# Kernel optimization log

Hardware: AMD Instinct MI355X
Metric: run time of the kernel (lower is better)

Reference implementation:

```python
import jax, jax.numpy as jnp
import numpy as np

B, S, DIM, H = 2, 1024, 512, 8
HD = DIM // H          # head_dim = 64
EPS = 1e-5
W_SCALE = 0.02         # keep activations stable (relu(gate)^2 downstream)


def causal_fft_conv(filters, x):
    """filters: [S, H]; x: [b, h, s, d]. Linear (full) convolution along s,
    truncated to the first s samples — identical to
    jax.scipy.signal.convolve(filter, seq, method='fft')[:s] per (h, d)."""
    s = x.shape[2]
    n = 2 * s  # >= 2s-1, enough for linear convolution
    f = jnp.fft.rfft(filters.T, n=n, axis=-1)          # [h, nf]
    xf = jnp.fft.rfft(x, n=n, axis=2)                  # [b, h, nf, d]
    y = jnp.fft.irfft(xf * f[None, :, :, None], n=n, axis=2)
    return y[:, :, :s, :]


def setup_inputs() -> dict:
    key = jax.random.key(0)
    ks = jax.random.split(key, 8)
    inp = {
        "x": jax.random.normal(ks[0], (B, S, DIM), dtype=jnp.float32),
        "spectral_basis": jax.random.normal(ks[1], (S, H), dtype=jnp.float32),
        "wq_w": jax.random.normal(ks[2], (DIM, DIM), dtype=jnp.float32) * W_SCALE,
        "wq_b": jnp.zeros((DIM,), jnp.float32),
        "wk_w": jax.random.normal(ks[3], (DIM, DIM), dtype=jnp.float32) * W_SCALE,
        "wk_b": jnp.zeros((DIM,), jnp.float32),
        "wv_w": jax.random.normal(ks[4], (DIM, DIM), dtype=jnp.float32) * W_SCALE,
        "wv_b": jnp.zeros((DIM,), jnp.float32),
        "wo_w": jax.random.normal(ks[5], (DIM, DIM), dtype=jnp.float32) * W_SCALE,
        "wo_b": jnp.zeros((DIM,), jnp.float32),
        "gate_w": jax.random.normal(ks[6], (HD * HD, 1), dtype=jnp.float32) * W_SCALE,
        "gate_b": jnp.zeros((1,), jnp.float32),
    }
    return inp


def reference(x, spectral_basis, wq_w, wq_b, wk_w, wk_b, wv_w, wv_b,
              wo_w, wo_b, gate_w, gate_b):
    b, s, dim = x.shape
    h = spectral_basis.shape[1]
    hd = dim // h

    def proj(w, bias):
        return (x @ w + bias).reshape(b, s, h, hd).transpose(0, 2, 1, 3)  # [b,h,s,d]

    q = proj(wq_w, wq_b)
    k = proj(wk_w, wk_b) / jnp.sqrt(jnp.asarray(hd, x.dtype))
    v = proj(wv_w, wv_b)

    k = causal_fft_conv(spectral_basis, k)
    v = causal_fft_conv(spectral_basis, v)

    # Outer-product state per step: [b, h, s, d, e]
    Z = jnp.einsum('bhsd,bhse->bhsde', v, k)

    # gate_proj: Dense(1) over flattened (d, e)
    gl = jnp.einsum('bhsde,de->bhs', Z, gate_w.reshape(hd, hd)) + gate_b[0]
    gates = jax.nn.relu(gl) ** 2 + EPS                 # [b, h, s]
    gates = gates[..., None, None]                     # [b, h, s, 1, 1]

    # Associative scan with (+, +) == cumulative sums along s
    cum_gZ = jnp.cumsum(gates * Z, axis=2)             # [b, h, s, d, e]
    cum_g = jnp.cumsum(gates, axis=2)                  # [b, h, s, 1, 1]
    attn = cum_gZ / (cum_g + EPS)

    out = jnp.einsum('bhsd,bhsde->bhse', q, attn)      # [b, h, s, e]
    nrm = jnp.linalg.norm(out, axis=3, keepdims=True)
    out = out / jnp.maximum(nrm, EPS)
    out = out.transpose(0, 2, 1, 3).reshape(b, s, dim)
    return out @ wo_w + wo_b
```

## Files before the change

kernel.cpp:

```cpp
#include <hip/hip_runtime.h>
#include <math.h>

#define B 2
#define S 1024
#define DIM 512
#define H 8
#define HD 64
#define EPS 1e-5f

typedef __attribute__((ext_vector_type(8))) short bf16x8;
typedef __attribute__((ext_vector_type(4))) float f32x4;
typedef unsigned short u16;

__device__ inline u16 f2bf(float f) {
    unsigned int u = __float_as_uint(f);
    return (u16)((u + 0x7FFF + ((u >> 16) & 1)) >> 16);
}
__device__ inline float bf2f(u16 v) {
    return __uint_as_float(((unsigned int)v) << 16);
}
__device__ inline void split2(float x, u16* hi, u16* lo) {
    u16 h = f2bf(x);
    *hi = h;
    *lo = f2bf(x - bf2f(h));
}
#define MFMA16(a, b, c) __builtin_amdgcn_mfma_f32_16x16x32_bf16((a), (b), (c), 0, 0, 0)

__global__ void xconv_k(const float* __restrict__ x, u16* __restrict__ xh, u16* __restrict__ xl) {
    int i = blockIdx.x * 256 + threadIdx.x;
    float4 v = ((const float4*)x)[i];
    ushort4 h, l;
    split2(v.x, &h.x, &l.x); split2(v.y, &h.y, &l.y);
    split2(v.z, &h.z, &l.z); split2(v.w, &h.w, &l.w);
    ((ushort4*)xh)[i] = h; ((ushort4*)xl)[i] = l;
}

__global__ void wconv_k(const float* __restrict__ wq, const float* __restrict__ wk,
                        const float* __restrict__ wv, const float* __restrict__ wo,
                        u16* __restrict__ wqkvh, u16* __restrict__ wqkvl,
                        u16* __restrict__ woh, u16* __restrict__ wol) {
    int z = blockIdx.z;
    const float* src = (z == 0) ? wq : (z == 1) ? wk : (z == 2) ? wv : wo;
    u16* dh = (z < 3) ? (wqkvh + (size_t)z * 512 * 512) : woh;
    u16* dl = (z < 3) ? (wqkvl + (size_t)z * 512 * 512) : wol;
    int k0 = blockIdx.x * 64, n0 = blockIdx.y * 64;
    int tid = threadIdx.x;
    __shared__ float T[64][65];
    #pragma unroll
    for (int p = 0; p < 16; ++p) {
        int i = tid + 256 * p; int r = i >> 6, c = i & 63;
        T[r][c] = src[(k0 + r) * 512 + n0 + c];
    }
    __syncthreads();
    #pragma unroll
    for (int p = 0; p < 16; ++p) {
        int i = tid + 256 * p; int r = i >> 6, c = i & 63;
        size_t di = (size_t)(n0 + r) * 512 + k0 + c;
        split2(T[c][r], &dh[di], &dl[di]);
    }
}

__global__ void toep_build(const float* __restrict__ filt,
                           u16* __restrict__ Th, u16* __restrict__ Tl) {
    int h = blockIdx.x, delta = blockIdx.y;
    int tid = threadIdx.x;
    size_t base = ((size_t)h * 16 + delta) << 12;
    #pragma unroll
    for (int p = 0; p < 16; ++p) {
        int i = tid + 256 * p;
        int t = i >> 6, s = i & 63;
        int idx = delta * 64 + t - s;
        float v = (idx >= 0 && idx < S) ? filt[idx * H + h] : 0.f;
        split2(v, &Th[base + i], &Tl[base + i]);
    }
}

__global__ void zero_k(float* __restrict__ a) {
    int i = blockIdx.x * 256 + threadIdx.x;
    ((float4*)a)[i] = make_float4(0.f, 0.f, 0.f, 0.f);
}

__global__ void qkv_gemm(const u16* __restrict__ Ah, const u16* __restrict__ Al,
                         const u16* __restrict__ Bh, const u16* __restrict__ Bl,
                         const float* __restrict__ bq, const float* __restrict__ bk,
                         const float* __restrict__ bv,
                         u16* __restrict__ qh, u16* __restrict__ ql,
                         u16* __restrict__ kth, u16* __restrict__ ktl,
                         u16* __restrict__ vth, u16* __restrict__ vtl) {
    const int K = 512;
    __shared__ __align__(16) u16 Ash[64][72], Asl[64][72], Bsh[64][72], Bsl[64][72];
    int tid = threadIdx.x, w = tid >> 6, l = tid & 63;
    int m0 = blockIdx.x * 64, n0 = blockIdx.y * 64;
    f32x4 acc[4] = {};
    for (int k0 = 0; k0 < K; k0 += 64) {
        #pragma unroll
        for (int p = 0; p < 2; ++p) {
            int i = tid + 256 * p; int r = i >> 3, c8 = (i & 7) * 8;
            *(bf16x8*)&Ash[r][c8] = *(const bf16x8*)&Ah[(size_t)(m0 + r) * K + k0 + c8];
            *(bf16x8*)&Asl[r][c8] = *(const bf16x8*)&Al[(size_t)(m0 + r) * K + k0 + c8];
            *(bf16x8*)&Bsh[r][c8] = *(const bf16x8*)&Bh[(size_t)(n0 + r) * K + k0 + c8];
            *(bf16x8*)&Bsl[r][c8] = *(const bf16x8*)&Bl[(size_t)(n0 + r) * K + k0 + c8];
        }
        __syncthreads();
        #pragma unroll
        for (int kc = 0; kc < 2; ++kc) {
            int ar = 16 * w + (l & 15), ac = kc * 32 + (l >> 4) * 8;
            bf16x8 ah = *(const bf16x8*)&Ash[ar][ac];
            bf16x8 al = *(const bf16x8*)&Asl[ar][ac];
            #pragma unroll
            for (int cf = 0; cf < 4; ++cf) {
                int br = cf * 16 + (l & 15);
                bf16x8 bh_ = *(const bf16x8*)&Bsh[br][ac];
                bf16x8 bl_ = *(const bf16x8*)&Bsl[br][ac];
                acc[cf] = MFMA16(ah, bh_, acc[cf]);
                acc[cf] = MFMA16(ah, bl_, acc[cf]);
                acc[cf] = MFMA16(al, bh_, acc[cf]);
            }
        }
        __syncthreads();
    }
    #pragma unroll
    for (int cf = 0; cf < 4; ++cf) {
        #pragma unroll
        for (int r = 0; r < 4; ++r) {
            int m = m0 + 16 * w + 4 * (l >> 4) + r;
            int n = n0 + 16 * cf + (l & 15);
            int bb = m >> 10, s = m & 1023;
            int which = n >> 9, nn = n & 511;
            int hh = nn >> 6, d = nn & 63;
            int bh = bb * 8 + hh;
            float val = acc[cf][r];
            if (which == 0) {
                val += bq[nn];
                size_t di = ((size_t)bh * 1024 + s) * 64 + d;
                split2(val, &qh[di], &ql[di]);
            } else if (which == 1) {
                val = (val + bk[nn]) * 0.125f;
                size_t di = ((size_t)bh * 64 + d) * 1024 + s;
                split2(val, &kth[di], &ktl[di]);
            } else {
                val += bv[nn];
                size_t di = ((size_t)bh * 64 + d) * 1024 + s;
                split2(val, &vth[di], &vtl[di]);
            }
        }
    }
}

#define NCH 4
#define CHW 4
__global__ void conv_part(const u16* __restrict__ kth, const u16* __restrict__ ktl,
                          const u16* __restrict__ vth, const u16* __restrict__ vtl,
                          const u16* __restrict__ Th, const u16* __restrict__ Tl,
                          float* __restrict__ Kacc, float* __restrict__ Vacc) {
    int tb = blockIdx.x, bh = blockIdx.y, ch = blockIdx.z;
    int h = bh & 7;
    int sb0 = ch * CHW;
    if (sb0 > tb) return;
    int sb1 = min(sb0 + CHW, tb + 1);
    int tid = threadIdx.x, w = tid >> 6, l = tid & 63;
    __shared__ __align__(16) u16 Ash[64][72], Asl[64][72];
    __shared__ __align__(16) u16 Ksh[64][72], Ksl[64][72], Vsh[64][72], Vsl[64][72];
    f32x4 aK[4] = {}, aV[4] = {};
    const size_t base = (size_t)bh * 64 * 1024;
    for (int sb = sb0; sb < sb1; ++sb) {
        size_t tbase = ((size_t)h * 16 + (tb - sb)) << 12;
        #pragma unroll
        for (int p = 0; p < 2; ++p) {
            int i = tid + 256 * p; int r = i >> 3, c8 = (i & 7) * 8;
            *(bf16x8*)&Ash[r][c8] = *(const bf16x8*)&Th[tbase + r * 64 + c8];
            *(bf16x8*)&Asl[r][c8] = *(const bf16x8*)&Tl[tbase + r * 64 + c8];
            *(bf16x8*)&Ksh[r][c8] = *(const bf16x8*)&kth[base + r * 1024 + sb * 64 + c8];
            *(bf16x8*)&Ksl[r][c8] = *(const bf16x8*)&ktl[base + r * 1024 + sb * 64 + c8];
            *(bf16x8*)&Vsh[r][c8] = *(const bf16x8*)&vth[base + r * 1024 + sb * 64 + c8];
            *(bf16x8*)&Vsl[r][c8] = *(const bf16x8*)&vtl[base + r * 1024 + sb * 64 + c8];
        }
        __syncthreads();
        #pragma unroll
        for (int kc = 0; kc < 2; ++kc) {
            int ar = 16 * w + (l & 15), ac = kc * 32 + (l >> 4) * 8;
            bf16x8 ah = *(const bf16x8*)&Ash[ar][ac];
            bf16x8 al = *(const bf16x8*)&Asl[ar][ac];
            #pragma unroll
            for (int cf = 0; cf < 4; ++cf) {
                int br = cf * 16 + (l & 15);
                bf16x8 kh8 = *(const bf16x8*)&Ksh[br][ac];
                bf16x8 kl8 = *(const bf16x8*)&Ksl[br][ac];
                bf16x8 vh8 = *(const bf16x8*)&Vsh[br][ac];
                bf16x8 vl8 = *(const bf16x8*)&Vsl[br][ac];
                aK[cf] = MFMA16(ah, kh8, aK[cf]);
                aK[cf] = MFMA16(ah, kl8, aK[cf]);
                aK[cf] = MFMA16(al, kh8, aK[cf]);
                aV[cf] = MFMA16(ah, vh8, aV[cf]);
                aV[cf] = MFMA16(ah, vl8, aV[cf]);
                aV[cf] = MFMA16(al, vh8, aV[cf]);
            }
        }
        __syncthreads();
    }
    #pragma unroll
    for (int cf = 0; cf < 4; ++cf) {
        #pragma unroll
        for (int r = 0; r < 4; ++r) {
            int tl_ = 16 * w + 4 * (l >> 4) + r;
            int d = cf * 16 + (l & 15);
            size_t oi = ((size_t)bh * 1024 + tb * 64 + tl_) * 64 + d;
            atomicAdd(&Kacc[oi], aK[cf][r]);
            atomicAdd(&Vacc[oi], aV[cf][r]);
        }
    }
}

__global__ void conv_fin(const float* __restrict__ Kacc, const float* __restrict__ Vacc,
                         const float* __restrict__ gw, const float* __restrict__ gb,
                         u16* __restrict__ kcth, u16* __restrict__ kctl,
                         u16* __restrict__ vcrh, u16* __restrict__ vcrl,
                         u16* __restrict__ vcth, u16* __restrict__ vctl,
                         float* __restrict__ g) {
    int sc = blockIdx.x, bh = blockIdx.y;
    int tid = threadIdx.x, tx = tid & 63, ty = tid >> 6;
    __shared__ float Kt[64][65], Vt[64][65], G[64][65];
    for (int i = tid; i < 4096; i += 256) {
        int r = i >> 6, c = i & 63;
        G[r][c] = gw[i];
        Kt[r][c] = Kacc[(((size_t)bh * 1024) + sc * 64 + r) * 64 + c];
        Vt[r][c] = Vacc[(((size_t)bh * 1024) + sc * 64 + r) * 64 + c];
    }
    __syncthreads();
    float gbias = gb[0];
    #pragma unroll
    for (int it = 0; it < 16; ++it) {
        int sl = it * 4 + ty;
        float t = 0.f;
        #pragma unroll
        for (int e = 0; e < 64; ++e) t += G[tx][e] * Kt[sl][e];
        float p = Vt[sl][tx] * t;
        #pragma unroll
        for (int off = 32; off >= 1; off >>= 1) p += __shfl_xor(p, off);
        if (tx == 0) { float gg = fmaxf(p + gbias, 0.f); g[(size_t)bh * 1024 + sc * 64 + sl] = gg * gg + EPS; }
    }
    #pragma unroll
    for (int it = 0; it < 16; ++it) {
        int r = it * 4 + ty;
        size_t ri = ((size_t)bh * 1024 + sc * 64 + r) * 64 + tx;
        split2(Vt[r][tx], &vcrh[ri], &vcrl[ri]);
    }
    #pragma unroll
    for (int it = 0; it < 16; ++it) {
        int d = it * 4 + ty;
        size_t ti = ((size_t)bh * 64 + d) * 1024 + sc * 64 + tx;
        split2(Kt[tx][d], &kcth[ti], &kctl[ti]);
        split2(Vt[tx][d], &vcth[ti], &vctl[ti]);
    }
}

__global__ void scan_k(const float* __restrict__ g, float* __restrict__ cumg) {
    int bh = blockIdx.x; int tid = threadIdx.x;
    __shared__ float a0[1024], a1[1024];
    for (int i = tid; i < 1024; i += 256) a0[i] = g[(size_t)bh * 1024 + i];
    float *sp = a0, *dp = a1;
    for (int off = 1; off < 1024; off <<= 1) {
        __syncthreads();
        for (int i = tid; i < 1024; i += 256) dp[i] = sp[i] + (i >= off ? sp[i - off] : 0.f);
        float* tmp = sp; sp = dp; dp = tmp;
    }
    __syncthreads();
    for (int i = tid; i < 1024; i += 256) cumg[(size_t)bh * 1024 + i] = sp[i];
}

__global__ void states_mfma(const u16* __restrict__ kcth, const u16* __restrict__ kctl,
                            const u16* __restrict__ vcth, const u16* __restrict__ vctl,
                            const float* __restrict__ g, float* __restrict__ Mst) {
    int j = blockIdx.x, bh = blockIdx.y;
    int tid = threadIdx.x, w = tid >> 6, l = tid & 63;
    __shared__ __align__(16) u16 Ash[64][72], Asl[64][72], Bsh[64][72], Bsl[64][72];
    __shared__ float gs[64];
    if (tid < 64) gs[tid] = g[(size_t)bh * 1024 + j * 64 + tid];
    __syncthreads();
    #pragma unroll
    for (int p = 0; p < 2; ++p) {
        int i = tid + 256 * p; int r = i >> 3, c8 = (i & 7) * 8;
        bf16x8 kh8 = *(const bf16x8*)&kcth[((size_t)bh * 64 + r) * 1024 + j * 64 + c8];
        bf16x8 kl8 = *(const bf16x8*)&kctl[((size_t)bh * 64 + r) * 1024 + j * 64 + c8];
        #pragma unroll
        for (int q = 0; q < 8; ++q) {
            float f = (bf2f((u16)kh8[q]) + bf2f((u16)kl8[q])) * gs[c8 + q];
            split2(f, &Ash[r][c8 + q], &Asl[r][c8 + q]);
        }
        *(bf16x8*)&Bsh[r][c8] = *(const bf16x8*)&vcth[((size_t)bh * 64 + r) * 1024 + j * 64 + c8];
        *(bf16x8*)&Bsl[r][c8] = *(const bf16x8*)&vctl[((size_t)bh * 64 + r) * 1024 + j * 64 + c8];
    }
    __syncthreads();
    f32x4 acc[4] = {};
    #pragma unroll
    for (int kc = 0; kc < 2; ++kc) {
        int ar = 16 * w + (l & 15), ac = kc * 32 + (l >> 4) * 8;
        bf16x8 ah = *(const bf16x8*)&Ash[ar][ac];
        bf16x8 al = *(const bf16x8*)&Asl[ar][ac];
        #pragma unroll
        for (int cf = 0; cf < 4; ++cf) {
            int br = cf * 16 + (l & 15);
            bf16x8 bh_ = *(const bf16x8*)&Bsh[br][ac];
            bf16x8 bl_ = *(const bf16x8*)&Bsl[br][ac];
            acc[cf] = MFMA16(ah, bh_, acc[cf]);
            acc[cf] = MFMA16(ah, bl_, acc[cf]);
            acc[cf] = MFMA16(al, bh_, acc[cf]);
        }
    }
    #pragma unroll
    for (int cf = 0; cf < 4; ++cf) {
        #pragma unroll
        for (int r = 0; r < 4; ++r) {
            int e = 16 * w + 4 * (l >> 4) + r;
            int d = cf * 16 + (l & 15);
            Mst[(((size_t)bh * 16 + j) * 64 + e) * 64 + d] = acc[cf][r];
        }
    }
}

__global__ void state_prefix(const float* __restrict__ Mst,
                             u16* __restrict__ ph, u16* __restrict__ pl) {
    int bh = blockIdx.x;
    int pos = blockIdx.y * 256 + threadIdx.x;
    float run = 0.f;
    #pragma unroll
    for (int j = 0; j < 16; ++j) {
        size_t idx = ((size_t)bh * 16 + j) * 4096 + pos;
        split2(run, &ph[idx], &pl[idx]);
        run += Mst[idx];
    }
}

__global__ void attn_mfma(const u16* __restrict__ qh, const u16* __restrict__ ql,
                          const u16* __restrict__ pexh, const u16* __restrict__ pexl,
                          const u16* __restrict__ vcrh, const u16* __restrict__ vcrl,
                          const u16* __restrict__ kcth, const u16* __restrict__ kctl,
                          const float* __restrict__ g, const float* __restrict__ cumg,
                          u16* __restrict__ yh, u16* __restrict__ yl) {
    int tb = blockIdx.x, bh = blockIdx.y;
    int b = bh >> 3, h = bh & 7;
    int tid = threadIdx.x, w = tid >> 6, l = tid & 63;
    __shared__ __align__(16) u16 buf[6][64][72];
    __shared__ float gl_s[64], cg_s[64];
    #pragma unroll
    for (int p = 0; p < 2; ++p) {
        int i = tid + 256 * p; int r = i >> 3, c8 = (i & 7) * 8;
        size_t rowi = ((size_t)bh * 1024 + tb * 64 + r) * 64 + c8;
        size_t pexi = (((size_t)bh * 16 + tb) * 64 + r) * 64 + c8;
        *(bf16x8*)&buf[0][r][c8] = *(const bf16x8*)&qh[rowi];
        *(bf16x8*)&buf[1][r][c8] = *(const bf16x8*)&ql[rowi];
        *(bf16x8*)&buf[2][r][c8] = *(const bf16x8*)&pexh[pexi];
        *(bf16x8*)&buf[3][r][c8] = *(const bf16x8*)&pexl[pexi];
        *(bf16x8*)&buf[4][r][c8] = *(const bf16x8*)&vcrh[rowi];
        *(bf16x8*)&buf[5][r][c8] = *(const bf16x8*)&vcrl[rowi];
    }
    if (tid < 64) {
        gl_s[tid] = g[(size_t)bh * 1024 + tb * 64 + tid];
        cg_s[tid] = cumg[(size_t)bh * 1024 + tb * 64 + tid];
    }
    __syncthreads();
    f32x4 o[4] = {}, sc[4] = {};
    #pragma unroll
    for (int kc = 0; kc < 2; ++kc) {
        int ar = 16 * w + (l & 15), ac = kc * 32 + (l >> 4) * 8;
        bf16x8 ah = *(const bf16x8*)&buf[0][ar][ac];
        bf16x8 al = *(const bf16x8*)&buf[1][ar][ac];
        #pragma unroll
        for (int cf = 0; cf < 4; ++cf) {
            int br = cf * 16 + (l & 15);
            bf16x8 bph = *(const bf16x8*)&buf[2][br][ac];
            bf16x8 bpl = *(const bf16x8*)&buf[3][br][ac];
            bf16x8 bvh = *(const bf16x8*)&buf[4][br][ac];
            bf16x8 bvl = *(const bf16x8*)&buf[5][br][ac];
            o[cf] = MFMA16(ah, bph, o[cf]);
            o[cf] = MFMA16(ah, bpl, o[cf]);
            o[cf] = MFMA16(al, bph, o[cf]);
            sc[cf] = MFMA16(ah, bvh, sc[cf]);
            sc[cf] = MFMA16(ah, bvl, sc[cf]);
            sc[cf] = MFMA16(al, bvh, sc[cf]);
        }
    }
    __syncthreads();
    #pragma unroll
    for (int cf = 0; cf < 4; ++cf) {
        int s = cf * 16 + (l & 15);
        float gsv = gl_s[s];
        #pragma unroll
        for (int r = 0; r < 4; ++r) {
            int t = 16 * w + 4 * (l >> 4) + r;
            float v = (s <= t) ? sc[cf][r] * gsv : 0.f;
            split2(v, &buf[2][t][s], &buf[3][t][s]);
        }
    }
    #pragma unroll
    for (int p = 0; p < 2; ++p) {
        int i = tid + 256 * p; int r = i >> 3, c8 = (i & 7) * 8;
        size_t ti = ((size_t)bh * 64 + r) * 1024 + tb * 64 + c8;
        *(bf16x8*)&buf[4][r][c8] = *(const bf16x8*)&kcth[ti];
        *(bf16x8*)&buf[5][r][c8] = *(const bf16x8*)&kctl[ti];
    }
    __syncthreads();
    #pragma unroll
    for (int kc = 0; kc < 2; ++kc) {
        int ar = 16 * w + (l & 15), ac = kc * 32 + (l >> 4) * 8;
        bf16x8 ah = *(const bf16x8*)&buf[2][ar][ac];
        bf16x8 al = *(const bf16x8*)&buf[3][ar][ac];
        #pragma unroll
        for (int cf = 0; cf < 4; ++cf) {
            int br = cf * 16 + (l & 15);
            bf16x8 bh_ = *(const bf16x8*)&buf[4][br][ac];
            bf16x8 bl_ = *(const bf16x8*)&buf[5][br][ac];
            o[cf] = MFMA16(ah, bh_, o[cf]);
            o[cf] = MFMA16(ah, bl_, o[cf]);
            o[cf] = MFMA16(al, bh_, o[cf]);
        }
    }
    #pragma unroll
    for (int r = 0; r < 4; ++r) {
        int tl_ = 16 * w + 4 * (l >> 4) + r;
        float inv = 1.f / (cg_s[tl_] + EPS);
        float vv[4]; float sq = 0.f;
        #pragma unroll
        for (int cf = 0; cf < 4; ++cf) { vv[cf] = o[cf][r] * inv; sq += vv[cf] * vv[cf]; }
        #pragma unroll
        for (int off = 1; off < 16; off <<= 1) sq += __shfl_xor(sq, off);
        float scale = 1.f / fmaxf(sqrtf(sq), EPS);
        int tg = tb * 64 + tl_;
        #pragma unroll
        for (int cf = 0; cf < 4; ++cf) {
            int e = cf * 16 + (l & 15);
            size_t yi = ((size_t)b * 1024 + tg) * 512 + h * 64 + e;
            split2(vv[cf] * scale, &yh[yi], &yl[yi]);
        }
    }
}

__global__ void out_gemm(const u16* __restrict__ Ah, const u16* __restrict__ Al,
                         const u16* __restrict__ Bh, const u16* __restrict__ Bl,
                         const float* __restrict__ bias, float* __restrict__ out) {
    const int K = 512, N = 512;
    __shared__ __align__(16) u16 Ash[64][72], Asl[64][72], Bsh[64][72], Bsl[64][72];
    int tid = threadIdx.x, w = tid >> 6, l = tid & 63;
    int m0 = blockIdx.x * 64, n0 = blockIdx.y * 64;
    f32x4 acc[4] = {};
    for (int k0 = 0; k0 < K; k0 += 64) {
        #pragma unroll
        for (int p = 0; p < 2; ++p) {
            int i = tid + 256 * p; int r = i >> 3, c8 = (i & 7) * 8;
            *(bf16x8*)&Ash[r][c8] = *(const bf16x8*)&Ah[(size_t)(m0 + r) * K + k0 + c8];
            *(bf16x8*)&Asl[r][c8] = *(const bf16x8*)&Al[(size_t)(m0 + r) * K + k0 + c8];
            *(bf16x8*)&Bsh[r][c8] = *(const bf16x8*)&Bh[(size_t)(n0 + r) * K + k0 + c8];
            *(bf16x8*)&Bsl[r][c8] = *(const bf16x8*)&Bl[(size_t)(n0 + r) * K + k0 + c8];
        }
        __syncthreads();
        #pragma unroll
        for (int kc = 0; kc < 2; ++kc) {
            int ar = 16 * w + (l & 15), ac = kc * 32 + (l >> 4) * 8;
            bf16x8 ah = *(const bf16x8*)&Ash[ar][ac];
            bf16x8 al = *(const bf16x8*)&Asl[ar][ac];
            #pragma unroll
            for (int cf = 0; cf < 4; ++cf) {
                int br = cf * 16 + (l & 15);
                bf16x8 bh_ = *(const bf16x8*)&Bsh[br][ac];
                bf16x8 bl_ = *(const bf16x8*)&Bsl[br][ac];
                acc[cf] = MFMA16(ah, bh_, acc[cf]);
                acc[cf] = MFMA16(ah, bl_, acc[cf]);
                acc[cf] = MFMA16(al, bh_, acc[cf]);
            }
        }
        __syncthreads();
    }
    #pragma unroll
    for (int cf = 0; cf < 4; ++cf) {
        #pragma unroll
        for (int r = 0; r < 4; ++r) {
            int m = m0 + 16 * w + 4 * (l >> 4) + r;
            int n = n0 + 16 * cf + (l & 15);
            out[(size_t)m * N + n] = acc[cf][r] + bias[n];
        }
    }
}

extern "C" void kernel_launch(void* const* d_in, const int* in_sizes, int n_in,
                              void* d_out, int out_size, void* d_ws, size_t ws_size,
                              hipStream_t stream) {
    const float* x    = (const float*)d_in[0];
    const float* sbas = (const float*)d_in[1];
    const float* wq_w = (const float*)d_in[2];
    const float* wq_b = (const float*)d_in[3];
    const float* wk_w = (const float*)d_in[4];
    const float* wk_b = (const float*)d_in[5];
    const float* wv_w = (const float*)d_in[6];
    const float* wv_b = (const float*)d_in[7];
    const float* wo_w = (const float*)d_in[8];
    const float* wo_b = (const float*)d_in[9];
    const float* gw   = (const float*)d_in[10];
    const float* gb   = (const float*)d_in[11];
    float* out = (float*)d_out;

    char* p = (char*)d_ws;
    auto carve = [&](size_t bytes) { char* r = p; p += (bytes + 255) & ~(size_t)255; return r; };
    const size_t T2 = (size_t)2048 * 512 * 2;
    u16* xh = (u16*)carve(T2);      u16* xl = (u16*)carve(T2);
    u16* wqkvh = (u16*)carve((size_t)1536 * 512 * 2);
    u16* wqkvl = (u16*)carve((size_t)1536 * 512 * 2);
    u16* woh = (u16*)carve((size_t)512 * 512 * 2);
    u16* wol = (u16*)carve((size_t)512 * 512 * 2);
    u16* qh_ = (u16*)carve(T2);     u16* ql_ = (u16*)carve(T2);
    u16* kth_ = (u16*)carve(T2);    u16* ktl_ = (u16*)carve(T2);
    u16* vth_ = (u16*)carve(T2);    u16* vtl_ = (u16*)carve(T2);
    u16* Tth = (u16*)carve((size_t)8 * 16 * 4096 * 2);
    u16* Ttl = (u16*)carve((size_t)8 * 16 * 4096 * 2);
    float* Kacc = (float*)carve((size_t)16 * 1024 * 64 * 4);
    float* Vacc = (float*)carve((size_t)16 * 1024 * 64 * 4);
    u16* kcth_ = (u16*)carve(T2);   u16* kctl_ = (u16*)carve(T2);
    u16* vcrh_ = (u16*)carve(T2);   u16* vcrl_ = (u16*)carve(T2);
    u16* vcth_ = (u16*)carve(T2);   u16* vctl_ = (u16*)carve(T2);
    float* gbuf = (float*)carve((size_t)16 * 1024 * 4);
    float* cumg = (float*)carve((size_t)16 * 1024 * 4);
    float* Mst  = (float*)carve((size_t)16 * 16 * 4096 * 4);
    u16* pexh_ = (u16*)carve(T2);   u16* pexl_ = (u16*)carve(T2);
    u16* yh_ = (u16*)carve(T2);     u16* yl_ = (u16*)carve(T2);

    xconv_k<<<1024, 256, 0, stream>>>(x, xh, xl);
    wconv_k<<<dim3(8, 8, 4), 256, 0, stream>>>(wq_w, wk_w, wv_w, wo_w, wqkvh, wqkvl, woh, wol);
    toep_build<<<dim3(8, 16), 256, 0, stream>>>(sbas, Tth, Ttl);
    zero_k<<<1024, 256, 0, stream>>>(Kacc);
    zero_k<<<1024, 256, 0, stream>>>(Vacc);
    qkv_gemm<<<dim3(32, 24), 256, 0, stream>>>(xh, xl, wqkvh, wqkvl, wq_b, wk_b, wv_b,
                                               qh_, ql_, kth_, ktl_, vth_, vtl_);
    conv_part<<<dim3(16, 16, NCH), 256, 0, stream>>>(kth_, ktl_, vth_, vtl_, Tth, Ttl, Kacc, Vacc);
    conv_fin<<<dim3(16, 16), 256, 0, stream>>>(Kacc, Vacc, gw, gb,
                                               kcth_, kctl_, vcrh_, vcrl_, vcth_, vctl_, gbuf);
    scan_k<<<16, 256, 0, stream>>>(gbuf, cumg);
    states_mfma<<<dim3(16, 16), 256, 0, stream>>>(kcth_, kctl_, vcth_, vctl_, gbuf, Mst);
    state_prefix<<<dim3(16, 16), 256, 0, stream>>>(Mst, pexh_, pexl_);
    attn_mfma<<<dim3(16, 16), 256, 0, stream>>>(qh_, ql_, pexh_, pexl_, vcrh_, vcrl_,
                                                kcth_, kctl_, gbuf, cumg, yh_, yl_);
    out_gemm<<<dim3(32, 8), 256, 0, stream>>>(yh_, yl_, woh, wol, wo_b, out);
}
```

Baseline: 213.1 us.

## Fuse prep kernels, add 128x128 direct-to-LDS GEMMs, compact conv grid, warp-shuffle scan

Merges the x, weight and Toeplitz conversion kernels into one launch and replaces the two zero kernels with a single memset. The QKV and output GEMMs become one templated kernel with 128x128 tiles, direct global-to-LDS loads and an XOR-swizzled LDS layout, with the three split-bf16 products run as separate K segments. conv_part gets a compact grid that skips empty causal blocks and uses the same direct-load swizzle. The scan moves to warp shuffles. Larger tiles cut reloads but give fewer blocks (192 and 64) on a big GPU, so occupancy may drop.

```diff
diff --git a/kernel.cpp b/kernel.cpp
--- a/kernel.cpp
+++ b/kernel.cpp
@@ -11,6 +11,7 @@
 typedef __attribute__((ext_vector_type(8))) short bf16x8;
 typedef __attribute__((ext_vector_type(4))) float f32x4;
 typedef unsigned short u16;
+typedef unsigned int u32;
 
 __device__ inline u16 f2bf(float f) {
     unsigned int u = __float_as_uint(f);
@@ -26,183 +27,210 @@
 }
 #define MFMA16(a, b, c) __builtin_amdgcn_mfma_f32_16x16x32_bf16((a), (b), (c), 0, 0, 0)
 
-__global__ void xconv_k(const float* __restrict__ x, u16* __restrict__ xh, u16* __restrict__ xl) {
-    int i = blockIdx.x * 256 + threadIdx.x;
-    float4 v = ((const float4*)x)[i];
-    ushort4 h, l;
-    split2(v.x, &h.x, &l.x); split2(v.y, &h.y, &l.y);
-    split2(v.z, &h.z, &l.z); split2(v.w, &h.w, &l.w);
-    ((ushort4*)xh)[i] = h; ((ushort4*)xl)[i] = l;
-}
-
-__global__ void wconv_k(const float* __restrict__ wq, const float* __restrict__ wk,
-                        const float* __restrict__ wv, const float* __restrict__ wo,
-                        u16* __restrict__ wqkvh, u16* __restrict__ wqkvl,
-                        u16* __restrict__ woh, u16* __restrict__ wol) {
-    int z = blockIdx.z;
-    const float* src = (z == 0) ? wq : (z == 1) ? wk : (z == 2) ? wv : wo;
-    u16* dh = (z < 3) ? (wqkvh + (size_t)z * 512 * 512) : woh;
-    u16* dl = (z < 3) ? (wqkvl + (size_t)z * 512 * 512) : wol;
-    int k0 = blockIdx.x * 64, n0 = blockIdx.y * 64;
-    int tid = threadIdx.x;
+__device__ inline void gl16(const void* g, void* l) {
+    __builtin_amdgcn_global_load_lds((const __attribute__((address_space(1))) u32*)g,
+                                     (__attribute__((address_space(3))) u32*)l, 16, 0, 0);
+}
+
+__global__ void prep_k(const float* __restrict__ x,
+                       const float* __restrict__ wq, const float* __restrict__ wk,
+                       const float* __restrict__ wv, const float* __restrict__ wo,
+                       const float* __restrict__ filt,
+                       u16* __restrict__ xh, u16* __restrict__ xl,
+                       u16* __restrict__ wqkvh, u16* __restrict__ wqkvl,
+                       u16* __restrict__ woh, u16* __restrict__ wol,
+                       u16* __restrict__ Th, u16* __restrict__ Tl) {
+    int bid = blockIdx.x, tid = threadIdx.x;
     __shared__ float T[64][65];
-    #pragma unroll
-    for (int p = 0; p < 16; ++p) {
-        int i = tid + 256 * p; int r = i >> 6, c = i & 63;
-        T[r][c] = src[(k0 + r) * 512 + n0 + c];
-    }
-    __syncthreads();
-    #pragma unroll
-    for (int p = 0; p < 16; ++p) {
-        int i = tid + 256 * p; int r = i >> 6, c = i & 63;
-        size_t di = (size_t)(n0 + r) * 512 + k0 + c;
-        split2(T[c][r], &dh[di], &dl[di]);
-    }
-}
-
-__global__ void toep_build(const float* __restrict__ filt,
-                           u16* __restrict__ Th, u16* __restrict__ Tl) {
-    int h = blockIdx.x, delta = blockIdx.y;
-    int tid = threadIdx.x;
-    size_t base = ((size_t)h * 16 + delta) << 12;
-    #pragma unroll
-    for (int p = 0; p < 16; ++p) {
-        int i = tid + 256 * p;
-        int t = i >> 6, s = i & 63;
-        int idx = delta * 64 + t - s;
-        float v = (idx >= 0 && idx < S) ? filt[idx * H + h] : 0.f;
-        split2(v, &Th[base + i], &Tl[base + i]);
-    }
-}
-
-__global__ void zero_k(float* __restrict__ a) {
-    int i = blockIdx.x * 256 + threadIdx.x;
-    ((float4*)a)[i] = make_float4(0.f, 0.f, 0.f, 0.f);
-}
-
-__global__ void qkv_gemm(const u16* __restrict__ Ah, const u16* __restrict__ Al,
-                         const u16* __restrict__ Bh, const u16* __restrict__ Bl,
-                         const float* __restrict__ bq, const float* __restrict__ bk,
-                         const float* __restrict__ bv,
-                         u16* __restrict__ qh, u16* __restrict__ ql,
-                         u16* __restrict__ kth, u16* __restrict__ ktl,
-                         u16* __restrict__ vth, u16* __restrict__ vtl) {
-    const int K = 512;
-    __shared__ __align__(16) u16 Ash[64][72], Asl[64][72], Bsh[64][72], Bsl[64][72];
-    int tid = threadIdx.x, w = tid >> 6, l = tid & 63;
-    int m0 = blockIdx.x * 64, n0 = blockIdx.y * 64;
-    f32x4 acc[4] = {};
-    for (int k0 = 0; k0 < K; k0 += 64) {
-        #pragma unroll
-        for (int p = 0; p < 2; ++p) {
-            int i = tid + 256 * p; int r = i >> 3, c8 = (i & 7) * 8;
-            *(bf16x8*)&Ash[r][c8] = *(const bf16x8*)&Ah[(size_t)(m0 + r) * K + k0 + c8];
-            *(bf16x8*)&Asl[r][c8] = *(const bf16x8*)&Al[(size_t)(m0 + r) * K + k0 + c8];
-            *(bf16x8*)&Bsh[r][c8] = *(const bf16x8*)&Bh[(size_t)(n0 + r) * K + k0 + c8];
-            *(bf16x8*)&Bsl[r][c8] = *(const bf16x8*)&Bl[(size_t)(n0 + r) * K + k0 + c8];
+    if (bid < 1024) {
+        int i = bid * 256 + tid;
+        float4 v = ((const float4*)x)[i];
+        ushort4 h, l;
+        split2(v.x, &h.x, &l.x); split2(v.y, &h.y, &l.y);
+        split2(v.z, &h.z, &l.z); split2(v.w, &h.w, &l.w);
+        ((ushort4*)xh)[i] = h; ((ushort4*)xl)[i] = l;
+    } else if (bid < 1280) {
+        int q = bid - 1024;
+        int z = q >> 6, rem = q & 63;
+        int k0 = (rem >> 3) * 64, n0 = (rem & 7) * 64;
+        const float* src = (z == 0) ? wq : (z == 1) ? wk : (z == 2) ? wv : wo;
+        u16* dh = (z < 3) ? (wqkvh + (size_t)z * 512 * 512) : woh;
+        u16* dl = (z < 3) ? (wqkvl + (size_t)z * 512 * 512) : wol;
+        #pragma unroll
+        for (int p = 0; p < 16; ++p) {
+            int i = tid + 256 * p; int r = i >> 6, c = i & 63;
+            T[r][c] = src[(k0 + r) * 512 + n0 + c];
         }
         __syncthreads();
         #pragma unroll
+        for (int p = 0; p < 16; ++p) {
+            int i = tid + 256 * p; int r = i >> 6, c = i & 63;
+            size_t di = (size_t)(n0 + r) * 512 + k0 + c;
+            split2(T[c][r], &dh[di], &dl[di]);
+        }
+    } else {
+        int q = bid - 1280;
+        int h = q >> 4, delta = q & 15;
+        size_t base = ((size_t)h * 16 + delta) << 12;
+        #pragma unroll
+        for (int p = 0; p < 16; ++p) {
+            int i = tid + 256 * p;
+            int t = i >> 6, s = i & 63;
+            int idx = delta * 64 + t - s;
+            float v = (idx >= 0 && idx < S) ? filt[idx * H + h] : 0.f;
+            split2(v, &Th[base + i], &Tl[base + i]);
+        }
+    }
+}
+
+template<int MODE>
+__global__ __launch_bounds__(256) void gemm3k(
+    const u16* __restrict__ Ah, const u16* __restrict__ Al,
+    const u16* __restrict__ Bh, const u16* __restrict__ Bl,
+    int N,
+    const float* __restrict__ b0, const float* __restrict__ b1, const float* __restrict__ b2,
+    float* __restrict__ outf,
+    u16* __restrict__ qh, u16* __restrict__ ql,
+    u16* __restrict__ kth, u16* __restrict__ ktl,
+    u16* __restrict__ vth, u16* __restrict__ vtl)
+{
+    __shared__ __align__(16) u16 As[128 * 64];
+    __shared__ __align__(16) u16 Bs[128 * 64];
+    int tid = threadIdx.x, wv = tid >> 6, l = tid & 63;
+    int wr = wv >> 1, wc = wv & 1;
+    int m0 = blockIdx.x * 128, n0 = blockIdx.y * 128;
+    f32x4 acc[4][4] = {};
+    for (int kv = 0; kv < 24; ++kv) {
+        int seg = kv >> 3, k0 = (kv & 7) * 64;
+        const u16* Ab = (seg < 2) ? Ah : Al;
+        const u16* Bb = (seg == 1) ? Bl : Bh;
+        __syncthreads();
+        #pragma unroll
+        for (int j = 0; j < 4; ++j) {
+            int row = (j * 4 + wv) * 8 + (l >> 3);
+            int csw = (l & 7) ^ (row & 7);
+            int lo = (j * 4 + wv) * 512;
+            gl16(Ab + (size_t)(m0 + row) * 512 + k0 + csw * 8, As + lo);
+            gl16(Bb + (size_t)(n0 + row) * 512 + k0 + csw * 8, Bs + lo);
+        }
+        __syncthreads();
+        #pragma unroll
         for (int kc = 0; kc < 2; ++kc) {
-            int ar = 16 * w + (l & 15), ac = kc * 32 + (l >> 4) * 8;
-            bf16x8 ah = *(const bf16x8*)&Ash[ar][ac];
-            bf16x8 al = *(const bf16x8*)&Asl[ar][ac];
+            bf16x8 a[4];
             #pragma unroll
-            for (int cf = 0; cf < 4; ++cf) {
-                int br = cf * 16 + (l & 15);
-                bf16x8 bh_ = *(const bf16x8*)&Bsh[br][ac];
-                bf16x8 bl_ = *(const bf16x8*)&Bsl[br][ac];
-                acc[cf] = MFMA16(ah, bh_, acc[cf]);
-                acc[cf] = MFMA16(ah, bl_, acc[cf]);
-                acc[cf] = MFMA16(al, bh_, acc[cf]);
+            for (int mi = 0; mi < 4; ++mi) {
+                int row = wr * 64 + mi * 16 + (l & 15);
+                int cb = (kc * 64 + (l >> 4) * 16) ^ ((row & 7) << 4);
+                a[mi] = *(const bf16x8*)((const char*)(As + row * 64) + cb);
             }
-        }
-        __syncthreads();
-    }
-    #pragma unroll
-    for (int cf = 0; cf < 4; ++cf) {
-        #pragma unroll
-        for (int r = 0; r < 4; ++r) {
-            int m = m0 + 16 * w + 4 * (l >> 4) + r;
-            int n = n0 + 16 * cf + (l & 15);
-            int bb = m >> 10, s = m & 1023;
-            int which = n >> 9, nn = n & 511;
-            int hh = nn >> 6, d = nn & 63;
-            int bh = bb * 8 + hh;
-            float val = acc[cf][r];
-            if (which == 0) {
-                val += bq[nn];
-                size_t di = ((size_t)bh * 1024 + s) * 64 + d;
-                split2(val, &qh[di], &ql[di]);
-            } else if (which == 1) {
-                val = (val + bk[nn]) * 0.125f;
-                size_t di = ((size_t)bh * 64 + d) * 1024 + s;
-                split2(val, &kth[di], &ktl[di]);
-            } else {
-                val += bv[nn];
-                size_t di = ((size_t)bh * 64 + d) * 1024 + s;
-                split2(val, &vth[di], &vtl[di]);
+            #pragma unroll
+            for (int ni = 0; ni < 4; ++ni) {
+                int rb = wc * 64 + ni * 16 + (l & 15);
+                int cbb = (kc * 64 + (l >> 4) * 16) ^ ((rb & 7) << 4);
+                bf16x8 b = *(const bf16x8*)((const char*)(Bs + rb * 64) + cbb);
+                #pragma unroll
+                for (int mi = 0; mi < 4; ++mi)
+                    acc[mi][ni] = MFMA16(a[mi], b, acc[mi][ni]);
             }
         }
     }
-}
-
-#define NCH 4
-#define CHW 4
-__global__ void conv_part(const u16* __restrict__ kth, const u16* __restrict__ ktl,
-                          const u16* __restrict__ vth, const u16* __restrict__ vtl,
-                          const u16* __restrict__ Th, const u16* __restrict__ Tl,
-                          float* __restrict__ Kacc, float* __restrict__ Vacc) {
-    int tb = blockIdx.x, bh = blockIdx.y, ch = blockIdx.z;
-    int h = bh & 7;
-    int sb0 = ch * CHW;
-    if (sb0 > tb) return;
-    int sb1 = min(sb0 + CHW, tb + 1);
-    int tid = threadIdx.x, w = tid >> 6, l = tid & 63;
-    __shared__ __align__(16) u16 Ash[64][72], Asl[64][72];
-    __shared__ __align__(16) u16 Ksh[64][72], Ksl[64][72], Vsh[64][72], Vsl[64][72];
+    #pragma unroll
+    for (int mi = 0; mi < 4; ++mi) {
+        #pragma unroll
+        for (int ni = 0; ni < 4; ++ni) {
+            #pragma unroll
+            for (int r = 0; r < 4; ++r) {
+                int m = m0 + wr * 64 + mi * 16 + 4 * (l >> 4) + r;
+                int n = n0 + wc * 64 + ni * 16 + (l & 15);
+                float val = acc[mi][ni][r];
+                if (MODE == 0) {
+                    outf[(size_t)m * N + n] = val + b0[n];
+                } else {
+                    int bb = m >> 10, s = m & 1023;
+                    int which = n >> 9, nn = n & 511;
+                    int hh = nn >> 6, d = nn & 63;
+                    int bh = bb * 8 + hh;
+                    if (which == 0) {
+                        val += b0[nn];
+                        size_t di = ((size_t)bh * 1024 + s) * 64 + d;
+                        split2(val, &qh[di], &ql[di]);
+                    } else if (which == 1) {
+                        val = (val + b1[nn]) * 0.125f;
+                        size_t di = ((size_t)bh * 64 + d) * 1024 + s;
+                        split2(val, &kth[di], &ktl[di]);
+                    } else {
+                        val += b2[nn];
+                        size_t di = ((size_t)bh * 64 + d) * 1024 + s;
+                        split2(val, &vth[di], &vtl[di]);
+                    }
+                }
+            }
+        }
+    }
+}
+
+__global__ __launch_bounds__(256) void conv_part(
+    const u16* __restrict__ kth, const u16* __restrict__ ktl,
+    const u16* __restrict__ vth, const u16* __restrict__ vtl,
+    const u16* __restrict__ Th, const u16* __restrict__ Tl,
+    float* __restrict__ Kacc, float* __restrict__ Vacc)
+{
+    int jid = blockIdx.x, bh = blockIdx.y, h = bh & 7;
+    int tb, ch;
+    if (jid < 4)       { tb = jid; ch = 0; }
+    else if (jid < 12) { int q = jid - 4;  tb = 4 + (q >> 1); ch = q & 1; }
+    else if (jid < 24) { int q = jid - 12; int d3 = q / 3; tb = 8 + d3; ch = q - 3 * d3; }
+    else               { int q = jid - 24; tb = 12 + (q >> 2); ch = q & 3; }
+    int sb0 = ch * 4, sb1 = min(sb0 + 4, tb + 1);
+    int tid = threadIdx.x, wv = tid >> 6, l = tid & 63;
+    __shared__ __align__(16) u16 Ash[4096], Asl[4096];
+    __shared__ __align__(16) u16 Ksh[4096], Ksl[4096], Vsh[4096], Vsl[4096];
     f32x4 aK[4] = {}, aV[4] = {};
     const size_t base = (size_t)bh * 64 * 1024;
     for (int sb = sb0; sb < sb1; ++sb) {
-        size_t tbase = ((size_t)h * 16 + (tb - sb)) << 12;
-        #pragma unroll
-        for (int p = 0; p < 2; ++p) {
-            int i = tid + 256 * p; int r = i >> 3, c8 = (i & 7) * 8;
-            *(bf16x8*)&Ash[r][c8] = *(const bf16x8*)&Th[tbase + r * 64 + c8];
-            *(bf16x8*)&Asl[r][c8] = *(const bf16x8*)&Tl[tbase + r * 64 + c8];
-            *(bf16x8*)&Ksh[r][c8] = *(const bf16x8*)&kth[base + r * 1024 + sb * 64 + c8];
-            *(bf16x8*)&Ksl[r][c8] = *(const bf16x8*)&ktl[base + r * 1024 + sb * 64 + c8];
-            *(bf16x8*)&Vsh[r][c8] = *(const bf16x8*)&vth[base + r * 1024 + sb * 64 + c8];
-            *(bf16x8*)&Vsl[r][c8] = *(const bf16x8*)&vtl[base + r * 1024 + sb * 64 + c8];
-        }
         __syncthreads();
-        #pragma unroll
-        for (int kc = 0; kc < 2; ++kc) {
-            int ar = 16 * w + (l & 15), ac = kc * 32 + (l >> 4) * 8;
-            bf16x8 ah = *(const bf16x8*)&Ash[ar][ac];
-            bf16x8 al = *(const bf16x8*)&Asl[ar][ac];
+        size_t tba = ((size_t)h * 16 + (tb - sb)) << 12;
+        #pragma unroll
+        for (int j = 0; j < 2; ++j) {
+            int row = (j * 4 + wv) * 8 + (l >> 3);
+            int csw = (l & 7) ^ (row & 7);
+            int lo = (j * 4 + wv) * 512;
+            gl16(Th + tba + row * 64 + csw * 8, Ash + lo);
+            gl16(Tl + tba + row * 64 + csw * 8, Asl + lo);
+            size_t gb = base + (size_t)row * 1024 + sb * 64 + csw * 8;
+            gl16(kth + gb, Ksh + lo);
+            gl16(ktl + gb, Ksl + lo);
+            gl16(vth + gb, Vsh + lo);
+            gl16(vtl + gb, Vsl + lo);
+        }
+        __syncthreads();
+        #pragma unroll
+        for (int seg = 0; seg < 3; ++seg) {
+            const u16* Ase = (seg < 2) ? Ash : Asl;
+            const u16* Kse = (seg == 1) ? Ksl : Ksh;
+            const u16* Vse = (seg == 1) ? Vsl : Vsh;
             #pragma unroll
-            for (int cf = 0; cf < 4; ++cf) {
-                int br = cf * 16 + (l & 15);
-                bf16x8 kh8 = *(const bf16x8*)&Ksh[br][ac];
-                bf16x8 kl8 = *(const bf16x8*)&Ksl[br][ac];
-                bf16x8 vh8 = *(const bf16x8*)&Vsh[br][ac];
-                bf16x8 vl8 = *(const bf16x8*)&Vsl[br][ac];
-                aK[cf] = MFMA16(ah, kh8, aK[cf]);
-                aK[cf] = MFMA16(ah, kl8, aK[cf]);
-                aK[cf] = MFMA16(al, kh8, aK[cf]);
-                aV[cf] = MFMA16(ah, vh8, aV[cf]);
-                aV[cf] = MFMA16(ah, vl8, aV[cf]);
-                aV[cf] = MFMA16(al, vh8, aV[cf]);
+            for (int kc = 0; kc < 2; ++kc) {
+                int ar = 16 * wv + (l & 15);
+                int acb = (kc * 64 + (l >> 4) * 16) ^ ((ar & 7) << 4);
+                bf16x8 a = *(const bf16x8*)((const char*)(Ase + ar * 64) + acb);
+                #pragma unroll
+                for (int cf = 0; cf < 4; ++cf) {
+                    int br = cf * 16 + (l & 15);
+                    int bcb = (kc * 64 + (l >> 4) * 16) ^ ((br & 7) << 4);
+                    bf16x8 bk = *(const bf16x8*)((const char*)(Kse + br * 64) + bcb);
+                    bf16x8 bv = *(const bf16x8*)((const char*)(Vse + br * 64) + bcb);
+                    aK[cf] = MFMA16(a, bk, aK[cf]);
+                    aV[cf] = MFMA16(a, bv, aV[cf]);
+                }
             }
         }
-        __syncthreads();
     }
     #pragma unroll
     for (int cf = 0; cf < 4; ++cf) {
         #pragma unroll
         for (int r = 0; r < 4; ++r) {
-            int tl_ = 16 * w + 4 * (l >> 4) + r;
+            int tl_ = 16 * wv + 4 * (l >> 4) + r;
             int d = cf * 16 + (l & 15);
             size_t oi = ((size_t)bh * 1024 + tb * 64 + tl_) * 64 + d;
             atomicAdd(&Kacc[oi], aK[cf][r]);
@@ -255,17 +283,22 @@
 }
 
 __global__ void scan_k(const float* __restrict__ g, float* __restrict__ cumg) {
-    int bh = blockIdx.x; int tid = threadIdx.x;
-    __shared__ float a0[1024], a1[1024];
-    for (int i = tid; i < 1024; i += 256) a0[i] = g[(size_t)bh * 1024 + i];
-    float *sp = a0, *dp = a1;
-    for (int off = 1; off < 1024; off <<= 1) {
-        __syncthreads();
-        for (int i = tid; i < 1024; i += 256) dp[i] = sp[i] + (i >= off ? sp[i - off] : 0.f);
-        float* tmp = sp; sp = dp; dp = tmp;
-    }
-    __syncthreads();
-    for (int i = tid; i < 1024; i += 256) cumg[(size_t)bh * 1024 + i] = sp[i];
+    int bh = blockIdx.x, tid = threadIdx.x, l = tid & 63, wv = tid >> 6;
+    __shared__ float wtot[4];
+    float4 v = ((const float4*)(g + (size_t)bh * 1024))[tid];
+    float p0 = v.x, p1 = p0 + v.y, p2 = p1 + v.z, p3 = p2 + v.w;
+    float t = p3, sc = t;
+    #pragma unroll
+    for (int off = 1; off < 64; off <<= 1) {
+        float u = __shfl_up(sc, off);
+        if (l >= off) sc += u;
+    }
+    if (l == 63) wtot[wv] = sc;
+    __syncthreads();
+    float bse = sc - t;
+    for (int w2 = 0; w2 < wv; ++w2) bse += wtot[w2];
+    float4 o = make_float4(bse + p0, bse + p1, bse + p2, bse + p3);
+    ((float4*)(cumg + (size_t)bh * 1024))[tid] = o;
 }
 
 __global__ void states_mfma(const u16* __restrict__ kcth, const u16* __restrict__ kctl,
@@ -431,52 +464,6 @@
             int e = cf * 16 + (l & 15);
             size_t yi = ((size_t)b * 1024 + tg) * 512 + h * 64 + e;
             split2(vv[cf] * scale, &yh[yi], &yl[yi]);
-        }
-    }
-}
-
-__global__ void out_gemm(const u16* __restrict__ Ah, const u16* __restrict__ Al,
-                         const u16* __restrict__ Bh, const u16* __restrict__ Bl,
-                         const float* __restrict__ bias, float* __restrict__ out) {
-    const int K = 512, N = 512;
-    __shared__ __align__(16) u16 Ash[64][72], Asl[64][72], Bsh[64][72], Bsl[64][72];
-    int tid = threadIdx.x, w = tid >> 6, l = tid & 63;
-    int m0 = blockIdx.x * 64, n0 = blockIdx.y * 64;
-    f32x4 acc[4] = {};
-    for (int k0 = 0; k0 < K; k0 += 64) {
-        #pragma unroll
-        for (int p = 0; p < 2; ++p) {
-            int i = tid + 256 * p; int r = i >> 3, c8 = (i & 7) * 8;
-            *(bf16x8*)&Ash[r][c8] = *(const bf16x8*)&Ah[(size_t)(m0 + r) * K + k0 + c8];
-            *(bf16x8*)&Asl[r][c8] = *(const bf16x8*)&Al[(size_t)(m0 + r) * K + k0 + c8];
-            *(bf16x8*)&Bsh[r][c8] = *(const bf16x8*)&Bh[(size_t)(n0 + r) * K + k0 + c8];
-            *(bf16x8*)&Bsl[r][c8] = *(const bf16x8*)&Bl[(size_t)(n0 + r) * K + k0 + c8];
-        }
-        __syncthreads();
-        #pragma unroll
-        for (int kc = 0; kc < 2; ++kc) {
-            int ar = 16 * w + (l & 15), ac = kc * 32 + (l >> 4) * 8;
-            bf16x8 ah = *(const bf16x8*)&Ash[ar][ac];
-            bf16x8 al = *(const bf16x8*)&Asl[ar][ac];
-            #pragma unroll
-            for (int cf = 0; cf < 4; ++cf) {
-                int br = cf * 16 + (l & 15);
-                bf16x8 bh_ = *(const bf16x8*)&Bsh[br][ac];
-                bf16x8 bl_ = *(const bf16x8*)&Bsl[br][ac];
-                acc[cf] = MFMA16(ah, bh_, acc[cf]);
-                acc[cf] = MFMA16(ah, bl_, acc[cf]);
-                acc[cf] = MFMA16(al, bh_, acc[cf]);
-            }
-        }
-        __syncthreads();
-    }
-    #pragma unroll
-    for (int cf = 0; cf < 4; ++cf) {
-        #pragma unroll
-        for (int r = 0; r < 4; ++r) {
-            int m = m0 + 16 * w + 4 * (l >> 4) + r;
-            int n = n0 + 16 * cf + (l & 15);
-            out[(size_t)m * N + n] = acc[cf][r] + bias[n];
         }
     }
 }
@@ -522,14 +509,13 @@
     u16* pexh_ = (u16*)carve(T2);   u16* pexl_ = (u16*)carve(T2);
     u16* yh_ = (u16*)carve(T2);     u16* yl_ = (u16*)carve(T2);
 
-    xconv_k<<<1024, 256, 0, stream>>>(x, xh, xl);
-    wconv_k<<<dim3(8, 8, 4), 256, 0, stream>>>(wq_w, wk_w, wv_w, wo_w, wqkvh, wqkvl, woh, wol);
-    toep_build<<<dim3(8, 16), 256, 0, stream>>>(sbas, Tth, Ttl);
-    zero_k<<<1024, 256, 0, stream>>>(Kacc);
-    zero_k<<<1024, 256, 0, stream>>>(Vacc);
-    qkv_gemm<<<dim3(32, 24), 256, 0, stream>>>(xh, xl, wqkvh, wqkvl, wq_b, wk_b, wv_b,
-                                               qh_, ql_, kth_, ktl_, vth_, vtl_);
-    conv_part<<<dim3(16, 16, NCH), 256, 0, stream>>>(kth_, ktl_, vth_, vtl_, Tth, Ttl, Kacc, Vacc);
+    hipMemsetAsync(Kacc, 0, (size_t)16 * 1024 * 64 * 4 * 2, stream);
+    prep_k<<<1408, 256, 0, stream>>>(x, wq_w, wk_w, wv_w, wo_w, sbas,
+                                     xh, xl, wqkvh, wqkvl, woh, wol, Tth, Ttl);
+    gemm3k<1><<<dim3(16, 12), 256, 0, stream>>>(xh, xl, wqkvh, wqkvl, 1536,
+                                                wq_b, wk_b, wv_b, nullptr,
+                                                qh_, ql_, kth_, ktl_, vth_, vtl_);
+    conv_part<<<dim3(40, 16), 256, 0, stream>>>(kth_, ktl_, vth_, vtl_, Tth, Ttl, Kacc, Vacc);
     conv_fin<<<dim3(16, 16), 256, 0, stream>>>(Kacc, Vacc, gw, gb,
                                                kcth_, kctl_, vcrh_, vcrl_, vcth_, vctl_, gbuf);
     scan_k<<<16, 256, 0, stream>>>(gbuf, cumg);
@@ -537,5 +523,7 @@
     state_prefix<<<dim3(16, 16), 256, 0, stream>>>(Mst, pexh_, pexl_);
     attn_mfma<<<dim3(16, 16), 256, 0, stream>>>(qh_, ql_, pexh_, pexl_, vcrh_, vcrl_,
                                                 kcth_, kctl_, gbuf, cumg, yh_, yl_);
-    out_gemm<<<dim3(32, 8), 256, 0, stream>>>(yh_, yl_, woh, wol, wo_b, out);
-}
+    gemm3k<0><<<dim3(16, 4), 256, 0, stream>>>(yh_, yl_, woh, wol, 512,
+                                               wo_b, nullptr, nullptr, out,
+                                               nullptr, nullptr, nullptr, nullptr, nullptr, nullptr);
+}
```

Measured after the change: 228.5 us. 7.2% more time.
